# Optimization experiments

Hardware: AMD Instinct MI355X
Metric: run time of the kernel (lower is better)

Reference implementation:

```python
import jax, jax.numpy as jnp
import numpy as np

B, I, O, G = 262144, 3, 64, 128


def setup_inputs() -> dict:
    key = jax.random.key(0)
    kx, kc = jax.random.split(key)
    x = jax.random.uniform(kx, (1, B, I), dtype=jnp.float32)  # coords in [0,1)
    coeffs = jax.random.normal(kc, (2, O, I, G), dtype=jnp.float32) / (
        np.float32(np.sqrt(I) * np.sqrt(G))
    )
    bias = jnp.zeros((1, O), dtype=jnp.float32)
    return {"x": x, "coeffs": coeffs, "bias": bias}


def reference(x, coeffs, bias):
    # x: (1, B, I); coeffs: (2, O, I, G); bias: (1, O)
    b, i = x.shape[1], x.shape[2]
    two, o, _, g = coeffs.shape
    k = jnp.arange(1, g + 1, dtype=x.dtype)          # (G,)
    kx = x.reshape(b, i, 1) * k                      # (B, I, G)
    cosf = jnp.cos(kx).reshape(b, i * g)             # (B, I*G)
    sinf = jnp.sin(kx).reshape(b, i * g)             # (B, I*G)
    w = coeffs.reshape(2, o, i * g)                  # (2, O, I*G)
    # sum over (input_dim, gridsize) fused as one GEMM per trig branch
    out = cosf @ w[0].T + sinf @ w[1].T + bias       # (B, O)
    return out
```

## Files before the change

### kernel.cpp

```cpp
#include <hip/hip_runtime.h>
#include <hip/hip_bf16.h>

typedef __attribute__((ext_vector_type(8))) short short8;
typedef __attribute__((ext_vector_type(4))) float f32x4;
typedef __attribute__((ext_vector_type(2))) float f32x2;
typedef __attribute__((ext_vector_type(4))) unsigned int u32x4;

#define NROWS   262144
#define ODIM    64
#define NBLOCKS 256
#define TPB     1024
#define INV2PI  0.15915494309189535f

__device__ __forceinline__ float cos2pi(float f){ float r; asm("v_cos_f32 %0, %1" : "=v"(r) : "v"(f)); return r; }
__device__ __forceinline__ float sin2pi(float f){ float r; asm("v_sin_f32 %0, %1" : "=v"(r) : "v"(f)); return r; }
__device__ __forceinline__ f32x2 pk_mul(f32x2 a, f32x2 b){
    f32x2 d; asm("v_pk_mul_f32 %0, %1, %2" : "=v"(d) : "v"(a), "v"(b)); return d; }
__device__ __forceinline__ f32x2 pk_fma(f32x2 a, f32x2 b, f32x2 c){
    f32x2 d; asm("v_pk_fma_f32 %0, %1, %2, %3" : "=v"(d) : "v"(a), "v"(b), "v"(c)); return d; }
__device__ __forceinline__ f32x2 pk_fms(f32x2 a, f32x2 b, f32x2 c){
    f32x2 d; asm("v_pk_fma_f32 %0, %1, %2, %3 neg_lo:[0,0,1] neg_hi:[0,0,1]"
                 : "=v"(d) : "v"(a), "v"(b), "v"(c)); return d; }
__device__ __forceinline__ unsigned pkbf(float lo, float hi){
    unsigned r; asm("v_cvt_pk_bf16_f32 %0, %1, %2" : "=v"(r) : "v"(lo), "v"(hi)); return r; }
__device__ __forceinline__ short8 as_s8(u32x4 v){ union{u32x4 u; short8 s;} x; x.u = v; return x.s; }
__device__ __forceinline__ short bf16_of(float f){
    union { __hip_bfloat16 h; short s; } u; u.h = __float2bfloat16(f); return u.s; }

extern "C" __global__ void __launch_bounds__(TPB, 4)
fourier_mfma(const float* __restrict__ x,
             const float* __restrict__ coeffs,
             const float* __restrict__ bias,
             float* __restrict__ out)
{
    __shared__ short8 Wlds[24 * 4 * 64];

    const int tid = threadIdx.x;

    for (int fl = tid; fl < 24*4*64; fl += TPB) {
        const int ks = fl >> 8;
        const int nt = (fl >> 6) & 3;
        const int ln = fl & 63;
        const int o  = nt*16 + (ln & 15);
        const int kg = ln >> 4;
        union { short8 v; short s[8]; } fr;
        #pragma unroll
        for (int h = 0; h < 2; ++h) {
            const int kb  = ks*32 + h*16;
            const int br  = (kb >= 384) ? 1 : 0;
            const int rem = kb - br*384;
            const int ii  = rem >> 7;
            const int g0  = (rem & 127) + kg*4;
            const float* wp = coeffs + (((br*ODIM + o)*3 + ii) << 7) + g0;
            #pragma unroll
            for (int j = 0; j < 4; ++j) fr.s[h*4 + j] = bf16_of(wp[j]);
        }
        Wlds[fl] = fr.v;
    }

    const int lane = tid & 63;
    const int wid  = tid >> 6;
    const int mrow = lane & 15;
    const int kgrp = lane >> 4;
    const float h0f = (float)(4*kgrp + 1);

    const int unit = blockIdx.x * 16 + wid;
    const int base = unit * 64;

    f32x2 xr[2][3];
    #pragma unroll
    for (int rg = 0; rg < 2; ++rg) {
        const int rowA = base + (rg*2 + 0)*16 + mrow;
        const int rowB = base + (rg*2 + 1)*16 + mrow;
        #pragma unroll
        for (int i = 0; i < 3; ++i)
            xr[rg][i] = (f32x2){ x[rowA*3 + i] * INV2PI, x[rowB*3 + i] * INV2PI };
    }
    float bcol[4];
    #pragma unroll
    for (int nt = 0; nt < 4; ++nt) bcol[nt] = bias[nt*16 + mrow];

    __syncthreads();

#define ANCHOR(RG, I) do {                                          \
    const f32x2 a = xr[RG][I];                                      \
    cv  = (f32x2){ cos2pi(a.x), cos2pi(a.y) };                      \
    sv  = (f32x2){ sin2pi(a.x), sin2pi(a.y) };                      \
    f32x2 t = (f32x2){ 16.f*a.x, 16.f*a.y };                        \
    t.x -= floorf(t.x); t.y -= floorf(t.y);                         \
    c16 = (f32x2){ cos2pi(t.x), cos2pi(t.y) };                      \
    s16 = (f32x2){ sin2pi(t.x), sin2pi(t.y) };                      \
    f32x2 u = (f32x2){ h0f*a.x, h0f*a.y };                          \
    u.x -= floorf(u.x); u.y -= floorf(u.y);                         \
    stc = (f32x2){ cos2pi(u.x), cos2pi(u.y) };                      \
    sts = (f32x2){ sin2pi(u.x), sin2pi(u.y) };                      \
} while (0)

#define HALF(D0, D1) do {                                           \
    const f32x2 c0 = stc, s0 = sts;                                 \
    const f32x2 c1 = pk_fms(c0, cv, pk_mul(s0, sv));                \
    const f32x2 s1 = pk_fma(s0, cv, pk_mul(c0, sv));                \
    FCA.D0 = pkbf(c0.x, c1.x);  FCB.D0 = pkbf(c0.y, c1.y);          \
    FSA.D0 = pkbf(s0.x, s1.x);  FSB.D0 = pkbf(s0.y, s1.y);          \
    const f32x2 c2 = pk_fms(c1, cv, pk_mul(s1, sv));                \
    const f32x2 s2 = pk_fma(s1, cv, pk_mul(c1, sv));                \
    const f32x2 c3 = pk_fms(c2, cv, pk_mul(s2, sv));                \
    const f32x2 s3 = pk_fma(s2, cv, pk_mul(c2, sv));                \
    FCA.D1 = pkbf(c2.x, c3.x);  FCB.D1 = pkbf(c2.y, c3.y);          \
    FSA.D1 = pkbf(s2.x, s3.x);  FSB.D1 = pkbf(s2.y, s3.y);          \
    const f32x2 nc = pk_fms(stc, c16, pk_mul(sts, s16));            \
    const f32x2 ns = pk_fma(stc, s16, pk_mul(sts, c16));            \
    stc = nc; sts = ns;                                             \
} while (0)

    #pragma unroll
    for (int rg = 0; rg < 2; ++rg) {
        f32x4 acc[2][4];
        #pragma unroll
        for (int rr = 0; rr < 2; ++rr)
            #pragma unroll
            for (int nt = 0; nt < 4; ++nt)
                acc[rr][nt] = (f32x4){0.f, 0.f, 0.f, 0.f};

        f32x2 cv, sv, c16, s16, stc, sts;

        #pragma unroll
        for (int kk = 0; kk < 12; ++kk) {
            short8 bc[4], bs[4];
            #pragma unroll
            for (int nt = 0; nt < 4; ++nt) {
                bc[nt] = Wlds[(kk*4 + nt)*64 + lane];
                bs[nt] = Wlds[((kk + 12)*4 + nt)*64 + lane];
            }

            if ((kk & 3) == 0) ANCHOR(rg, kk >> 2);

            u32x4 FCA, FCB, FSA, FSB;
            HALF(x, y);
            HALF(z, w);

            const short8 fAc = as_s8(FCA);
            const short8 fBc = as_s8(FCB);
            const short8 fAs = as_s8(FSA);
            const short8 fBs = as_s8(FSB);

            __builtin_amdgcn_s_setprio(1);
            #pragma unroll
            for (int nt = 0; nt < 4; ++nt)
                acc[0][nt] = __builtin_amdgcn_mfma_f32_16x16x32_bf16(fAc, bc[nt], acc[0][nt], 0, 0, 0);
            #pragma unroll
            for (int nt = 0; nt < 4; ++nt)
                acc[1][nt] = __builtin_amdgcn_mfma_f32_16x16x32_bf16(fBc, bc[nt], acc[1][nt], 0, 0, 0);
            #pragma unroll
            for (int nt = 0; nt < 4; ++nt)
                acc[0][nt] = __builtin_amdgcn_mfma_f32_16x16x32_bf16(fAs, bs[nt], acc[0][nt], 0, 0, 0);
            #pragma unroll
            for (int nt = 0; nt < 4; ++nt)
                acc[1][nt] = __builtin_amdgcn_mfma_f32_16x16x32_bf16(fBs, bs[nt], acc[1][nt], 0, 0, 0);
            __builtin_amdgcn_s_setprio(0);
        }

        #pragma unroll
        for (int rr = 0; rr < 2; ++rr) {
            const int row0 = base + (rg*2 + rr)*16 + kgrp*4;
            #pragma unroll
            for (int nt = 0; nt < 4; ++nt) {
                #pragma unroll
                for (int q = 0; q < 4; ++q) {
                    out[(row0 + q)*ODIM + nt*16 + mrow] = acc[rr][nt][q] + bcol[nt];
                }
            }
        }
    }
#undef HALF
#undef ANCHOR
}

extern "C" void kernel_launch(void* const* d_in, const int* in_sizes, int n_in,
                              void* d_out, int out_size, void* d_ws, size_t ws_size,
                              hipStream_t stream) {
    const float* x      = (const float*)d_in[0];
    const float* coeffs = (const float*)d_in[1];
    const float* bias   = (const float*)d_in[2];
    float* out = (float*)d_out;
    (void)in_sizes; (void)n_in; (void)out_size; (void)d_ws; (void)ws_size;
    hipLaunchKernelGGL(fourier_mfma, dim3(NBLOCKS), dim3(TPB), 0, stream, x, coeffs, bias, out);
}
```

Baseline: 41.68 us.

## Process all four row tiles per wave at once and double-buffer LDS weight loads

```diff
diff --git a/kernel.cpp b/kernel.cpp
--- a/kernel.cpp
+++ b/kernel.cpp
@@ -8,8 +8,8 @@
 
 #define NROWS   262144
 #define ODIM    64
-#define NBLOCKS 256
-#define TPB     1024
+#define NBLOCKS 512
+#define TPB     512
 #define INV2PI  0.15915494309189535f
 
 __device__ __forceinline__ float cos2pi(float f){ float r; asm("v_cos_f32 %0, %1" : "=v"(r) : "v"(f)); return r; }
@@ -27,7 +27,7 @@
 __device__ __forceinline__ short bf16_of(float f){
     union { __hip_bfloat16 h; short s; } u; u.h = __float2bfloat16(f); return u.s; }
 
-extern "C" __global__ void __launch_bounds__(TPB, 4)
+extern "C" __global__ void __launch_bounds__(TPB, 2)
 fourier_mfma(const float* __restrict__ x,
              const float* __restrict__ coeffs,
              const float* __restrict__ bias,
@@ -64,17 +64,17 @@
     const int kgrp = lane >> 4;
     const float h0f = (float)(4*kgrp + 1);
 
-    const int unit = blockIdx.x * 16 + wid;
+    const int unit = blockIdx.x * 8 + wid;
     const int base = unit * 64;
 
     f32x2 xr[2][3];
     #pragma unroll
-    for (int rg = 0; rg < 2; ++rg) {
-        const int rowA = base + (rg*2 + 0)*16 + mrow;
-        const int rowB = base + (rg*2 + 1)*16 + mrow;
+    for (int p = 0; p < 2; ++p) {
+        const int rowA = base + (2*p + 0)*16 + mrow;
+        const int rowB = base + (2*p + 1)*16 + mrow;
         #pragma unroll
         for (int i = 0; i < 3; ++i)
-            xr[rg][i] = (f32x2){ x[rowA*3 + i] * INV2PI, x[rowB*3 + i] * INV2PI };
+            xr[p][i] = (f32x2){ x[rowA*3 + i] * INV2PI, x[rowB*3 + i] * INV2PI };
     }
     float bcol[4];
     #pragma unroll
@@ -82,93 +82,104 @@
 
     __syncthreads();
 
-#define ANCHOR(RG, I) do {                                          \
-    const f32x2 a = xr[RG][I];                                      \
-    cv  = (f32x2){ cos2pi(a.x), cos2pi(a.y) };                      \
-    sv  = (f32x2){ sin2pi(a.x), sin2pi(a.y) };                      \
+#define ANCHOR(P, I) do {                                           \
+    const f32x2 a = xr[P][I];                                       \
+    cv[P]  = (f32x2){ cos2pi(a.x), cos2pi(a.y) };                   \
+    sv[P]  = (f32x2){ sin2pi(a.x), sin2pi(a.y) };                   \
     f32x2 t = (f32x2){ 16.f*a.x, 16.f*a.y };                        \
     t.x -= floorf(t.x); t.y -= floorf(t.y);                         \
-    c16 = (f32x2){ cos2pi(t.x), cos2pi(t.y) };                      \
-    s16 = (f32x2){ sin2pi(t.x), sin2pi(t.y) };                      \
+    c16[P] = (f32x2){ cos2pi(t.x), cos2pi(t.y) };                   \
+    s16[P] = (f32x2){ sin2pi(t.x), sin2pi(t.y) };                   \
     f32x2 u = (f32x2){ h0f*a.x, h0f*a.y };                          \
     u.x -= floorf(u.x); u.y -= floorf(u.y);                         \
-    stc = (f32x2){ cos2pi(u.x), cos2pi(u.y) };                      \
-    sts = (f32x2){ sin2pi(u.x), sin2pi(u.y) };                      \
+    stc[P] = (f32x2){ cos2pi(u.x), cos2pi(u.y) };                   \
+    sts[P] = (f32x2){ sin2pi(u.x), sin2pi(u.y) };                   \
 } while (0)
 
-#define HALF(D0, D1) do {                                           \
-    const f32x2 c0 = stc, s0 = sts;                                 \
-    const f32x2 c1 = pk_fms(c0, cv, pk_mul(s0, sv));                \
-    const f32x2 s1 = pk_fma(s0, cv, pk_mul(c0, sv));                \
-    FCA.D0 = pkbf(c0.x, c1.x);  FCB.D0 = pkbf(c0.y, c1.y);          \
-    FSA.D0 = pkbf(s0.x, s1.x);  FSB.D0 = pkbf(s0.y, s1.y);          \
-    const f32x2 c2 = pk_fms(c1, cv, pk_mul(s1, sv));                \
-    const f32x2 s2 = pk_fma(s1, cv, pk_mul(c1, sv));                \
-    const f32x2 c3 = pk_fms(c2, cv, pk_mul(s2, sv));                \
-    const f32x2 s3 = pk_fma(s2, cv, pk_mul(c2, sv));                \
-    FCA.D1 = pkbf(c2.x, c3.x);  FCB.D1 = pkbf(c2.y, c3.y);          \
-    FSA.D1 = pkbf(s2.x, s3.x);  FSB.D1 = pkbf(s2.y, s3.y);          \
-    const f32x2 nc = pk_fms(stc, c16, pk_mul(sts, s16));            \
-    const f32x2 ns = pk_fma(stc, s16, pk_mul(sts, c16));            \
-    stc = nc; sts = ns;                                             \
+#define HALF(P, D0, D1) do {                                        \
+    const f32x2 c0 = stc[P], s0 = sts[P];                           \
+    const f32x2 c1 = pk_fms(c0, cv[P], pk_mul(s0, sv[P]));          \
+    const f32x2 s1 = pk_fma(s0, cv[P], pk_mul(c0, sv[P]));          \
+    fCA[P].D0 = pkbf(c0.x, c1.x);  fCB[P].D0 = pkbf(c0.y, c1.y);    \
+    fSA[P].D0 = pkbf(s0.x, s1.x);  fSB[P].D0 = pkbf(s0.y, s1.y);    \
+    const f32x2 c2 = pk_fms(c1, cv[P], pk_mul(s1, sv[P]));          \
+    const f32x2 s2 = pk_fma(s1, cv[P], pk_mul(c1, sv[P]));          \
+    const f32x2 c3 = pk_fms(c2, cv[P], pk_mul(s2, sv[P]));          \
+    const f32x2 s3 = pk_fma(s2, cv[P], pk_mul(c2, sv[P]));          \
+    fCA[P].D1 = pkbf(c2.x, c3.x);  fCB[P].D1 = pkbf(c2.y, c3.y);    \
+    fSA[P].D1 = pkbf(s2.x, s3.x);  fSB[P].D1 = pkbf(s2.y, s3.y);    \
+    const f32x2 nc = pk_fms(stc[P], c16[P], pk_mul(sts[P], s16[P]));\
+    const f32x2 ns = pk_fma(stc[P], s16[P], pk_mul(sts[P], c16[P]));\
+    stc[P] = nc; sts[P] = ns;                                       \
 } while (0)
 
+    f32x4 acc[4][4];
     #pragma unroll
-    for (int rg = 0; rg < 2; ++rg) {
-        f32x4 acc[2][4];
+    for (int rt = 0; rt < 4; ++rt)
         #pragma unroll
-        for (int rr = 0; rr < 2; ++rr)
+        for (int nt = 0; nt < 4; ++nt)
+            acc[rt][nt] = (f32x4){0.f, 0.f, 0.f, 0.f};
+
+    f32x2 cv[2], sv[2], c16[2], s16[2], stc[2], sts[2];
+    short8 bc[2][4], bs[2][4];
+
+    #pragma unroll
+    for (int nt = 0; nt < 4; ++nt) {
+        bc[0][nt] = Wlds[(0*4 + nt)*64 + lane];
+        bs[0][nt] = Wlds[(12*4 + nt)*64 + lane];
+    }
+
+    #pragma unroll
+    for (int kk = 0; kk < 12; ++kk) {
+        const int cur = kk & 1;
+        if (kk < 11) {
+            #pragma unroll
+            for (int nt = 0; nt < 4; ++nt) {
+                bc[cur^1][nt] = Wlds[((kk+1)*4 + nt)*64 + lane];
+                bs[cur^1][nt] = Wlds[((kk+13)*4 + nt)*64 + lane];
+            }
+        }
+
+        if ((kk & 3) == 0) { ANCHOR(0, kk >> 2); ANCHOR(1, kk >> 2); }
+
+        u32x4 fCA[2], fCB[2], fSA[2], fSB[2];
+        HALF(0, x, y);  HALF(0, z, w);
+        HALF(1, x, y);  HALF(1, z, w);
+
+        __builtin_amdgcn_s_setprio(1);
+        #pragma unroll
+        for (int p = 0; p < 2; ++p) {
+            const short8 fA = as_s8(fCA[p]);
+            const short8 fB = as_s8(fCB[p]);
             #pragma unroll
             for (int nt = 0; nt < 4; ++nt)
-                acc[rr][nt] = (f32x4){0.f, 0.f, 0.f, 0.f};
-
-        f32x2 cv, sv, c16, s16, stc, sts;
-
-        #pragma unroll
-        for (int kk = 0; kk < 12; ++kk) {
-            short8 bc[4], bs[4];
-            #pragma unroll
-            for (int nt = 0; nt < 4; ++nt) {
-                bc[nt] = Wlds[(kk*4 + nt)*64 + lane];
-                bs[nt] = Wlds[((kk + 12)*4 + nt)*64 + lane];
-            }
-
-            if ((kk & 3) == 0) ANCHOR(rg, kk >> 2);
-
-            u32x4 FCA, FCB, FSA, FSB;
-            HALF(x, y);
-            HALF(z, w);
-
-            const short8 fAc = as_s8(FCA);
-            const short8 fBc = as_s8(FCB);
-            const short8 fAs = as_s8(FSA);
-            const short8 fBs = as_s8(FSB);
-
-            __builtin_amdgcn_s_setprio(1);
+                acc[2*p+0][nt] = __builtin_amdgcn_mfma_f32_16x16x32_bf16(fA, bc[cur][nt], acc[2*p+0][nt], 0, 0, 0);
             #pragma unroll
             for (int nt = 0; nt < 4; ++nt)
-                acc[0][nt] = __builtin_amdgcn_mfma_f32_16x16x32_bf16(fAc, bc[nt], acc[0][nt], 0, 0, 0);
+                acc[2*p+1][nt] = __builtin_amdgcn_mfma_f32_16x16x32_bf16(fB, bc[cur][nt], acc[2*p+1][nt], 0, 0, 0);
+        }
+        #pragma unroll
+        for (int p = 0; p < 2; ++p) {
+            const short8 fA = as_s8(fSA[p]);
+            const short8 fB = as_s8(fSB[p]);
             #pragma unroll
             for (int nt = 0; nt < 4; ++nt)
-                acc[1][nt] = __builtin_amdgcn_mfma_f32_16x16x32_bf16(fBc, bc[nt], acc[1][nt], 0, 0, 0);
+                acc[2*p+0][nt] = __builtin_amdgcn_mfma_f32_16x16x32_bf16(fA, bs[cur][nt], acc[2*p+0][nt], 0, 0, 0);
             #pragma unroll
             for (int nt = 0; nt < 4; ++nt)
-                acc[0][nt] = __builtin_amdgcn_mfma_f32_16x16x32_bf16(fAs, bs[nt], acc[0][nt], 0, 0, 0);
+                acc[2*p+1][nt] = __builtin_amdgcn_mfma_f32_16x16x32_bf16(fB, bs[cur][nt], acc[2*p+1][nt], 0, 0, 0);
+        }
+        __builtin_amdgcn_s_setprio(0);
+    }
+
+    #pragma unroll
+    for (int rt = 0; rt < 4; ++rt) {
+        const int row0 = base + rt*16 + kgrp*4;
+        #pragma unroll
+        for (int nt = 0; nt < 4; ++nt) {
             #pragma unroll
-            for (int nt = 0; nt < 4; ++nt)
-                acc[1][nt] = __builtin_amdgcn_mfma_f32_16x16x32_bf16(fBs, bs[nt], acc[1][nt], 0, 0, 0);
-            __builtin_amdgcn_s_setprio(0);
-        }
-
-        #pragma unroll
-        for (int rr = 0; rr < 2; ++rr) {
-            const int row0 = base + (rg*2 + rr)*16 + kgrp*4;
-            #pragma unroll
-            for (int nt = 0; nt < 4; ++nt) {
-                #pragma unroll
-                for (int q = 0; q < 4; ++q) {
-                    out[(row0 + q)*ODIM + nt*16 + mrow] = acc[rr][nt][q] + bcol[nt];
-                }
+            for (int q = 0; q < 4; ++q) {
+                out[(row0 + q)*ODIM + nt*16 + mrow] = acc[rt][nt][q] + bcol[nt];
             }
         }
     }
```

Result: slower. 47.46 us (+13.9%).
